# Performance work log

Hardware: AMD Instinct MI355X
Metric: run time of the kernel (lower is better)

The kernel has to match this reference:

```python
import jax, jax.numpy as jnp
from jax import lax
import numpy as np


def setup_inputs() -> dict:
    key = jax.random.key(0)
    k1, k2, k3, k4 = jax.random.split(key, 4)
    x = jax.random.normal(k1, (16, 128, 128, 128), dtype=jnp.float32)
    weight = jax.random.normal(k2, (128, 128, 3, 3), dtype=jnp.float32)      # ITPLConv.weight (d, c, kh, kw)
    depth_w = jax.random.normal(k3, (128,), dtype=jnp.float32)               # depthwise 1x1 conv weight (c,1,1,1) flattened
    point_w = jax.random.normal(k4, (128, 128), dtype=jnp.float32)           # pointwise 1x1 conv weight (out, in)
    return {"x": x, "weight": weight, "depth_w": depth_w, "point_w": point_w}


def reference(x, weight, depth_w, point_w):
    # ZeroPad2d(padding=1) on H and W
    xp = jnp.pad(x, ((0, 0), (0, 0), (1, 1), (1, 1)))
    # substract2: unfold(x) - x[:,:,:uh,:uw] broadcast, contracted with weight.
    # Algebraically: conv2d(xp, W, stride=1, VALID) - einsum(xp_crop, W.sum(kh,kw))
    conv = lax.conv_general_dilated(
        xp, weight, window_strides=(1, 1), padding="VALID",
        dimension_numbers=("NCHW", "OIHW", "NCHW"))
    uh, uw = conv.shape[2], conv.shape[3]
    wsum = jnp.sum(weight, axis=(2, 3))                      # (d, c)
    corr = jnp.einsum("nchw,dc->ndhw", xp[:, :, :uh, :uw], wsum)
    sub = conv - corr                                        # (n, d, uh, uw)
    # DWconv: depthwise 1x1 (per-channel scale) then pointwise 1x1
    y = sub * depth_w[None, :, None, None]
    out = jnp.einsum("nchw,oc->nohw", y, point_w)
    return out
```

## Files before the change

kernel.cpp:

```cpp
#include <hip/hip_runtime.h>
#include <hip/hip_bf16.h>


typedef __attribute__((ext_vector_type(8))) short bf16x8;
typedef __attribute__((ext_vector_type(4))) float f32x4;
typedef __attribute__((ext_vector_type(2))) unsigned int u32x2;

__device__ inline unsigned short f2bf(float f) {
    unsigned u = __builtin_bit_cast(unsigned, f);
    return (unsigned short)((u + 0x7FFFu + ((u >> 16) & 1u)) >> 16);
}

__device__ inline void gll16(const void* g, void* l) {
    __builtin_amdgcn_global_load_lds((const __attribute__((address_space(1))) void*)g,
                                     (__attribute__((address_space(3))) void*)l, 16, 0, 0);
}

__global__ void fuse_weights_bf16(const float* __restrict__ W,
                                  const float* __restrict__ dw,
                                  const float* __restrict__ P,
                                  unsigned short* __restrict__ w2b) {
    const int c = blockIdx.x;
    const int o = threadIdx.x;
    float acc[9];
#pragma unroll
    for (int t = 0; t < 9; ++t) acc[t] = 0.f;
    for (int d = 0; d < 128; ++d) {
        const float s = P[o * 128 + d] * dw[d];
        const float* wp = W + (size_t)(d * 128 + c) * 9;
        float tsum = 0.f;
#pragma unroll
        for (int t = 0; t < 9; ++t) {
            const float wv = wp[t];
            acc[t] = fmaf(s, wv, acc[t]);
            tsum += wv;
        }
        acc[0] = fmaf(-s, tsum, acc[0]);
    }
#pragma unroll
    for (int t = 0; t < 9; ++t)
        w2b[(t * 128 + o) * 128 + c] = f2bf(acc[t]);
}

__global__ __launch_bounds__(256) void to_nhwc_bf16(const float* __restrict__ x,
                                                    unsigned short* __restrict__ xb,
                                                    unsigned short* __restrict__ zrow) {
    __shared__ __attribute__((aligned(16))) unsigned ys[128 * 68];
    const int h = blockIdx.x, n = blockIdx.y, tid = (int)threadIdx.x;
    const int wv = tid >> 6, l = tid & 63;

#pragma unroll
    for (int i = 0; i < 4; ++i) {
        const int wh = (i & 1) * 64;
        const int CB0 = (2 * wv + (i >> 1)) * 16;
        const int c0 = CB0 + 4 * (l >> 4);
        const int w0 = wh + 4 * (l & 15);

        float4 v[4];
#pragma unroll
        for (int r = 0; r < 4; ++r)
            v[r] = *reinterpret_cast<const float4*>(
                x + ((((size_t)n * 128 + c0 + r) * 128 + h) * 128 + w0));

        const float* vf = reinterpret_cast<const float*>(v);
#pragma unroll
        for (int j = 0; j < 4; ++j) {
            unsigned u0 = (unsigned)f2bf(vf[0 * 4 + j]) | ((unsigned)f2bf(vf[1 * 4 + j]) << 16);
            unsigned u1 = (unsigned)f2bf(vf[2 * 4 + j]) | ((unsigned)f2bf(vf[3 * 4 + j]) << 16);
            u32x2 st; st[0] = u0; st[1] = u1;
            *reinterpret_cast<u32x2*>(&ys[(w0 + j) * 68 + (c0 >> 1)]) = st;
        }
    }
    __syncthreads();

#pragma unroll
    for (int k = 0; k < 8; ++k) {
        const int u = tid + 256 * k;
        const int c8 = u & 15, w = u >> 4;
        bf16x8 val = *reinterpret_cast<const bf16x8*>(
            reinterpret_cast<const unsigned short*>(ys) + w * 136 + c8 * 8);
        *reinterpret_cast<bf16x8*>(
            xb + ((((size_t)n * 128 + h) * 128 + w) * 128 + c8 * 8)) = val;
    }

    if (h == 0 && n == 0) {
        bf16x8 z = 0;
        for (int u = tid; u < 2048; u += 256)
            *reinterpret_cast<bf16x8*>(zrow + u * 8) = z;
    }
}

#define LDS_CHUNK (3 * 132 * 32)

__global__ __launch_bounds__(256, 2) void itpl_mfma_kernel(
    const unsigned short* __restrict__ xb,
    const unsigned short* __restrict__ w2b,
    const unsigned short* __restrict__ zrow,
    float* __restrict__ out) {
    __shared__ __attribute__((aligned(16))) unsigned short lds[2][LDS_CHUNK];

    const int bid = (int)blockIdx.x;
    const int lin = (bid & 7) * 256 + (bid >> 3);
    const int h = lin & 127, n = lin >> 7;

    const int tid = (int)threadIdx.x;
    const int l = tid & 63, wid = tid >> 6;
    const int wr = wid >> 1, wc = wid & 1;

    f32x4 acc[4][4];
#pragma unroll
    for (int i = 0; i < 4; ++i)
#pragma unroll
        for (int j = 0; j < 4; ++j) acc[i][j] = {0.f, 0.f, 0.f, 0.f};

    if (tid < 48) {
        const int slot = tid & 3, row = tid >> 2;
        const int buf = row / 6, rr = row % 6, r = rr >> 1, wi = (rr & 1) ? 129 : 0;
        bf16x8 z = 0;
        *reinterpret_cast<bf16x8*>(&lds[buf][(r * 132 + wi) * 32 + slot * 8]) = z;
    }

    const size_t nbase = (size_t)n * 128;

    auto stage = [&](int buf, int c0) {
        for (int s = wid * 6; s < wid * 6 + 6; ++s) {
            const int r = s >> 3, seg = s & 7;
            const int hr = h + r - 1;
            const int wl = seg * 16 + (l >> 2);
            const int wi = 1 + wl;
            const int q = (l & 3) ^ ((wi >> 1) & 3);
            const unsigned short* src;
            if ((unsigned)hr < 128u)
                src = xb + (((nbase + hr) * 128 + wl) * 128) + c0 + q * 8;
            else
                src = zrow + (wl * 128 + c0 + q * 8);
            gll16(src, (void*)&lds[buf][(r * 132 + 1 + seg * 16) * 32]);
        }
    };

    auto compute = [&](int buf, int c0) {
        const unsigned short* lb = &lds[buf][0];
#pragma unroll
        for (int r = 0; r < 3; ++r) {
            bf16x8 bfr[3][4];
#pragma unroll
            for (int tt = 0; tt < 3; ++tt)
#pragma unroll
                for (int ni = 0; ni < 4; ++ni) {
                    const int t = r * 3 + tt;
                    const int o = wc * 64 + ni * 16 + (l & 15);
                    bfr[tt][ni] = *reinterpret_cast<const bf16x8*>(
                        w2b + ((t * 128 + o) * 128 + c0 + (l >> 4) * 8));
                }
#pragma unroll
            for (int kw = 0; kw < 3; ++kw) {
                bf16x8 afr[4];
#pragma unroll
                for (int mi = 0; mi < 4; ++mi) {
                    const int wi = 1 + wr * 64 + mi * 16 + (l & 15) + kw - 1;
                    const int slot = (l >> 4) ^ ((wi >> 1) & 3);
                    afr[mi] = *reinterpret_cast<const bf16x8*>(
                        lb + (r * 132 + wi) * 32 + slot * 8);
                }
#pragma unroll
                for (int mi = 0; mi < 4; ++mi)
#pragma unroll
                    for (int ni = 0; ni < 4; ++ni)
                        acc[mi][ni] = __builtin_amdgcn_mfma_f32_16x16x32_bf16(
                            afr[mi], bfr[kw][ni], acc[mi][ni], 0, 0, 0);
            }
        }
    };

    stage(0, 0);
    __syncthreads();
#pragma unroll
    for (int k = 0; k < 4; ++k) {
        if (k < 3) stage((k + 1) & 1, (k + 1) * 32);
        compute(k & 1, k * 32);
        __syncthreads();
    }

    const size_t ob = (nbase * 128 + h) * 128;
#pragma unroll
    for (int mi = 0; mi < 4; ++mi) {
        const int w = wr * 64 + mi * 16 + (l >> 4) * 4;
#pragma unroll
        for (int ni = 0; ni < 4; ++ni) {
            const int o = wc * 64 + ni * 16 + (l & 15);
            *reinterpret_cast<f32x4*>(out + ob + (size_t)o * 128 * 128 + w) = acc[mi][ni];
        }
    }
}

#define CB 32
__global__ void fuse_weights_kernel(const float* __restrict__ W,
                                    const float* __restrict__ dw,
                                    const float* __restrict__ P,
                                    float* __restrict__ W2) {
    const int c = blockIdx.x;
    const int o = threadIdx.x;
    float acc[9];
#pragma unroll
    for (int t = 0; t < 9; ++t) acc[t] = 0.f;
    for (int d = 0; d < 128; ++d) {
        const float s = P[o * 128 + d] * dw[d];
        const float* wp = W + (size_t)(d * 128 + c) * 9;
        float tsum = 0.f;
#pragma unroll
        for (int t = 0; t < 9; ++t) {
            const float wv = wp[t];
            acc[t] = fmaf(s, wv, acc[t]);
            tsum += wv;
        }
        acc[0] = fmaf(-s, tsum, acc[0]);
    }
#pragma unroll
    for (int t = 0; t < 9; ++t) W2[(c * 9 + t) * 128 + o] = acc[t];
}

__global__ __launch_bounds__(256) void itpl_conv_kernel(const float* __restrict__ x,
                                                        const float* __restrict__ W2,
                                                        float* __restrict__ out) {
    __shared__ float xs[CB][3][132];
    const int h = blockIdx.x;
    const int n = blockIdx.y;
    const int tid = (int)threadIdx.x;
    const int pg = tid & 15;
    const int og = tid >> 4;
    float acc[8][8];
#pragma unroll
    for (int i = 0; i < 8; ++i)
#pragma unroll
        for (int p = 0; p < 8; ++p) acc[i][p] = 0.f;
    for (int c0 = 0; c0 < 128; c0 += CB) {
        __syncthreads();
        for (int g = tid; g < CB * 3 * 32; g += 256) {
            const int f4 = g & 31;
            const int row = g >> 5;
            const int r = row % 3;
            const int c = row / 3;
            const int hr = h + r - 1;
            float4 v = make_float4(0.f, 0.f, 0.f, 0.f);
            if ((unsigned)hr < 128u)
                v = *reinterpret_cast<const float4*>(
                    x + ((((size_t)n * 128 + c0 + c) * 128 + hr) * 128 + f4 * 4));
            float* dst = &xs[c][r][1 + f4 * 4];
            dst[0] = v.x; dst[1] = v.y; dst[2] = v.z; dst[3] = v.w;
        }
        if (tid < CB * 3) {
            const int r = tid % 3;
            const int c = tid / 3;
            xs[c][r][0] = 0.f;
            xs[c][r][129] = 0.f;
        }
        __syncthreads();
        for (int c = 0; c < CB; ++c) {
#pragma unroll
            for (int kh = 0; kh < 3; ++kh) {
                float xr[12];
                const float* xsp = &xs[c][kh][pg * 8];
                *reinterpret_cast<float4*>(&xr[0]) = *reinterpret_cast<const float4*>(xsp);
                *reinterpret_cast<float4*>(&xr[4]) = *reinterpret_cast<const float4*>(xsp + 4);
                *reinterpret_cast<float4*>(&xr[8]) = *reinterpret_cast<const float4*>(xsp + 8);
#pragma unroll
                for (int kw = 0; kw < 3; ++kw) {
                    const float* wp = W2 + (size_t)((c0 + c) * 9 + kh * 3 + kw) * 128 + og * 8;
                    float wv[8];
                    *reinterpret_cast<float4*>(&wv[0]) = *reinterpret_cast<const float4*>(wp);
                    *reinterpret_cast<float4*>(&wv[4]) = *reinterpret_cast<const float4*>(wp + 4);
#pragma unroll
                    for (int i = 0; i < 8; ++i)
#pragma unroll
                        for (int p = 0; p < 8; ++p)
                            acc[i][p] = fmaf(wv[i], xr[p + kw], acc[i][p]);
                }
            }
        }
    }
#pragma unroll
    for (int i = 0; i < 8; ++i) {
        float* op = out + ((((size_t)n * 128 + og * 8 + i) * 128 + h) * 128 + pg * 8);
        *reinterpret_cast<float4*>(op)     = make_float4(acc[i][0], acc[i][1], acc[i][2], acc[i][3]);
        *reinterpret_cast<float4*>(op + 4) = make_float4(acc[i][4], acc[i][5], acc[i][6], acc[i][7]);
    }
}

extern "C" void kernel_launch(void* const* d_in, const int* in_sizes, int n_in,
                              void* d_out, int out_size, void* d_ws, size_t ws_size,
                              hipStream_t stream) {
    const float* x  = (const float*)d_in[0];
    const float* W  = (const float*)d_in[1];
    const float* dw = (const float*)d_in[2];
    const float* P  = (const float*)d_in[3];
    float* out = (float*)d_out;

    const size_t XB_BYTES = 67108864ull;
    const size_t ZR_BYTES = 32768ull;
    const size_t W2B_BYTES = 294912ull;
    if (ws_size >= XB_BYTES + ZR_BYTES + W2B_BYTES) {
        unsigned short* xbw  = (unsigned short*)d_ws;
        unsigned short* zrow = (unsigned short*)((char*)d_ws + XB_BYTES);
        unsigned short* w2b  = (unsigned short*)((char*)d_ws + XB_BYTES + ZR_BYTES);
        fuse_weights_bf16<<<128, 128, 0, stream>>>(W, dw, P, w2b);
        to_nhwc_bf16<<<dim3(128, 16), 256, 0, stream>>>(x, xbw, zrow);
        itpl_mfma_kernel<<<2048, 256, 0, stream>>>(xbw, w2b, zrow, out);
    } else {
        float* W2 = (float*)d_ws;
        fuse_weights_kernel<<<128, 128, 0, stream>>>(W, dw, P, W2);
        itpl_conv_kernel<<<dim3(128, 16), 256, 0, stream>>>(x, W2, out);
    }
}
```

Before: 413.2 us.

## Merge prep kernels and retile MFMA conv to 512 threads with swapped operands

The weight-fusion and NHWC-conversion kernels are merged into one launch, and the weight fusion now stages W in shared memory and splits the reduction over d between two thread halves. The main MFMA kernel moves to 512 threads with 8 waves, each computing 64 output channels by 32 pixels, so the weight fragments become the A operand. Weights are stored in a layout grouped by 8 input channels so those fragment loads coalesce. This cuts launch overhead and per-wave register pressure to allow more waves in flight. The cost is output stores that become scalar strided writes along w instead of f32x4 vectors.

```diff
diff --git a/kernel.cpp b/kernel.cpp
--- a/kernel.cpp
+++ b/kernel.cpp
@@ -1,5 +1,4 @@
 #include <hip/hip_runtime.h>
-#include <hip/hip_bf16.h>
 
 
 typedef __attribute__((ext_vector_type(8))) short bf16x8;
@@ -16,85 +15,101 @@
                                      (__attribute__((address_space(3))) void*)l, 16, 0, 0);
 }
 
-__global__ void fuse_weights_bf16(const float* __restrict__ W,
-                                  const float* __restrict__ dw,
-                                  const float* __restrict__ P,
-                                  unsigned short* __restrict__ w2b) {
-    const int c = blockIdx.x;
-    const int o = threadIdx.x;
-    float acc[9];
-#pragma unroll
-    for (int t = 0; t < 9; ++t) acc[t] = 0.f;
-    for (int d = 0; d < 128; ++d) {
-        const float s = P[o * 128 + d] * dw[d];
-        const float* wp = W + (size_t)(d * 128 + c) * 9;
-        float tsum = 0.f;
-#pragma unroll
-        for (int t = 0; t < 9; ++t) {
-            const float wv = wp[t];
-            acc[t] = fmaf(s, wv, acc[t]);
-            tsum += wv;
-        }
-        acc[0] = fmaf(-s, tsum, acc[0]);
-    }
-#pragma unroll
-    for (int t = 0; t < 9; ++t)
-        w2b[(t * 128 + o) * 128 + c] = f2bf(acc[t]);
-}
-
-__global__ __launch_bounds__(256) void to_nhwc_bf16(const float* __restrict__ x,
-                                                    unsigned short* __restrict__ xb,
-                                                    unsigned short* __restrict__ zrow) {
-    __shared__ __attribute__((aligned(16))) unsigned ys[128 * 68];
-    const int h = blockIdx.x, n = blockIdx.y, tid = (int)threadIdx.x;
-    const int wv = tid >> 6, l = tid & 63;
-
-#pragma unroll
-    for (int i = 0; i < 4; ++i) {
-        const int wh = (i & 1) * 64;
-        const int CB0 = (2 * wv + (i >> 1)) * 16;
-        const int c0 = CB0 + 4 * (l >> 4);
-        const int w0 = wh + 4 * (l & 15);
-
-        float4 v[4];
-#pragma unroll
-        for (int r = 0; r < 4; ++r)
-            v[r] = *reinterpret_cast<const float4*>(
-                x + ((((size_t)n * 128 + c0 + r) * 128 + h) * 128 + w0));
-
-        const float* vf = reinterpret_cast<const float*>(v);
-#pragma unroll
-        for (int j = 0; j < 4; ++j) {
-            unsigned u0 = (unsigned)f2bf(vf[0 * 4 + j]) | ((unsigned)f2bf(vf[1 * 4 + j]) << 16);
-            unsigned u1 = (unsigned)f2bf(vf[2 * 4 + j]) | ((unsigned)f2bf(vf[3 * 4 + j]) << 16);
-            u32x2 st; st[0] = u0; st[1] = u1;
-            *reinterpret_cast<u32x2*>(&ys[(w0 + j) * 68 + (c0 >> 1)]) = st;
-        }
-    }
-    __syncthreads();
-
-#pragma unroll
-    for (int k = 0; k < 8; ++k) {
-        const int u = tid + 256 * k;
-        const int c8 = u & 15, w = u >> 4;
-        bf16x8 val = *reinterpret_cast<const bf16x8*>(
-            reinterpret_cast<const unsigned short*>(ys) + w * 136 + c8 * 8);
-        *reinterpret_cast<bf16x8*>(
-            xb + ((((size_t)n * 128 + h) * 128 + w) * 128 + c8 * 8)) = val;
-    }
-
-    if (h == 0 && n == 0) {
-        bf16x8 z = 0;
-        for (int u = tid; u < 2048; u += 256)
-            *reinterpret_cast<bf16x8*>(zrow + u * 8) = z;
+__global__ __launch_bounds__(256) void prep_kernel(
+    const float* __restrict__ x, const float* __restrict__ W,
+    const float* __restrict__ dw, const float* __restrict__ P,
+    unsigned short* __restrict__ xb, unsigned short* __restrict__ zrow,
+    unsigned short* __restrict__ w2f) {
+    __shared__ __attribute__((aligned(16))) unsigned smem[128 * 68];
+    const int bid = (int)blockIdx.x, tid = (int)threadIdx.x;
+
+    if (bid < 2048) {
+        const int h = bid & 127, n = bid >> 7;
+        const int wv = tid >> 6, l = tid & 63;
+#pragma unroll
+        for (int i = 0; i < 4; ++i) {
+            const int wh = (i & 1) * 64;
+            const int CB0 = (2 * wv + (i >> 1)) * 16;
+            const int c0 = CB0 + 4 * (l >> 4);
+            const int w0 = wh + 4 * (l & 15);
+            float4 v[4];
+#pragma unroll
+            for (int r = 0; r < 4; ++r)
+                v[r] = *reinterpret_cast<const float4*>(
+                    x + ((((size_t)n * 128 + c0 + r) * 128 + h) * 128 + w0));
+            const float* vf = reinterpret_cast<const float*>(v);
+#pragma unroll
+            for (int j = 0; j < 4; ++j) {
+                unsigned u0 = (unsigned)f2bf(vf[0 * 4 + j]) | ((unsigned)f2bf(vf[1 * 4 + j]) << 16);
+                unsigned u1 = (unsigned)f2bf(vf[2 * 4 + j]) | ((unsigned)f2bf(vf[3 * 4 + j]) << 16);
+                u32x2 st; st[0] = u0; st[1] = u1;
+                *reinterpret_cast<u32x2*>(&smem[(w0 + j) * 68 + (c0 >> 1)]) = st;
+            }
+        }
+        __syncthreads();
+#pragma unroll
+        for (int k = 0; k < 8; ++k) {
+            const int u = tid + 256 * k;
+            const int c8 = u & 15, w = u >> 4;
+            bf16x8 val = *reinterpret_cast<const bf16x8*>(
+                reinterpret_cast<const unsigned short*>(smem) + w * 136 + c8 * 8);
+            *reinterpret_cast<bf16x8*>(
+                xb + ((((size_t)n * 128 + h) * 128 + w) * 128 + c8 * 8)) = val;
+        }
+        if (h == 0 && n == 0) {
+            bf16x8 z = 0;
+            for (int u = tid; u < 2048; u += 256)
+                *reinterpret_cast<bf16x8*>(zrow + u * 8) = z;
+        }
+    } else {
+        const int c = bid - 2048;
+        float* Wl  = reinterpret_cast<float*>(smem);
+        float* red = reinterpret_cast<float*>(smem) + 1152;
+        for (int idx = tid; idx < 1152; idx += 256)
+            Wl[idx] = W[(size_t)((idx / 9) * 128 + c) * 9 + (idx % 9)];
+        __syncthreads();
+        const int t8 = tid >> 7, o = tid & 127;
+        float pr[64];
+#pragma unroll
+        for (int q = 0; q < 16; ++q)
+            *reinterpret_cast<float4*>(&pr[q * 4]) = *reinterpret_cast<const float4*>(
+                P + (size_t)o * 128 + t8 * 64 + q * 4);
+        float acc[9];
+#pragma unroll
+        for (int t = 0; t < 9; ++t) acc[t] = 0.f;
+        for (int dd = 0; dd < 64; ++dd) {
+            const int d = t8 * 64 + dd;
+            const float s = pr[dd] * dw[d];
+            const float* wp = Wl + d * 9;
+            float tsum = 0.f;
+#pragma unroll
+            for (int t = 0; t < 9; ++t) {
+                const float wv2 = wp[t];
+                acc[t] = fmaf(s, wv2, acc[t]);
+                tsum += wv2;
+            }
+            acc[0] = fmaf(-s, tsum, acc[0]);
+        }
+        if (t8 == 1) {
+#pragma unroll
+            for (int t = 0; t < 9; ++t) red[o * 10 + t] = acc[t];
+        }
+        __syncthreads();
+        if (t8 == 0) {
+#pragma unroll
+            for (int t = 0; t < 9; ++t) {
+                const float v = acc[t] + red[o * 10 + t];
+                w2f[(size_t)((t * 16 + (c >> 3)) * 128 + o) * 8 + (c & 7)] = f2bf(v);
+            }
+        }
     }
 }
 
 #define LDS_CHUNK (3 * 132 * 32)
 
-__global__ __launch_bounds__(256, 2) void itpl_mfma_kernel(
+__global__ __launch_bounds__(512, 6) void itpl_mfma_kernel(
     const unsigned short* __restrict__ xb,
-    const unsigned short* __restrict__ w2b,
+    const unsigned short* __restrict__ w2f,
     const unsigned short* __restrict__ zrow,
     float* __restrict__ out) {
     __shared__ __attribute__((aligned(16))) unsigned short lds[2][LDS_CHUNK];
@@ -105,13 +120,13 @@
 
     const int tid = (int)threadIdx.x;
     const int l = tid & 63, wid = tid >> 6;
-    const int wr = wid >> 1, wc = wid & 1;
-
-    f32x4 acc[4][4];
+    const int ws = wid & 3, wo = wid >> 2;
+
+    f32x4 acc[4][2];
 #pragma unroll
     for (int i = 0; i < 4; ++i)
 #pragma unroll
-        for (int j = 0; j < 4; ++j) acc[i][j] = {0.f, 0.f, 0.f, 0.f};
+        for (int j = 0; j < 2; ++j) acc[i][j] = {0.f, 0.f, 0.f, 0.f};
 
     if (tid < 48) {
         const int slot = tid & 3, row = tid >> 2;
@@ -123,7 +138,9 @@
     const size_t nbase = (size_t)n * 128;
 
     auto stage = [&](int buf, int c0) {
-        for (int s = wid * 6; s < wid * 6 + 6; ++s) {
+#pragma unroll
+        for (int i = 0; i < 3; ++i) {
+            const int s = wid * 3 + i;
             const int r = s >> 3, seg = s & 7;
             const int hr = h + r - 1;
             const int wl = seg * 16 + (l >> 2);
@@ -140,34 +157,33 @@
 
     auto compute = [&](int buf, int c0) {
         const unsigned short* lb = &lds[buf][0];
+        const int g0 = c0 >> 3;
 #pragma unroll
         for (int r = 0; r < 3; ++r) {
-            bf16x8 bfr[3][4];
-#pragma unroll
-            for (int tt = 0; tt < 3; ++tt)
-#pragma unroll
-                for (int ni = 0; ni < 4; ++ni) {
-                    const int t = r * 3 + tt;
-                    const int o = wc * 64 + ni * 16 + (l & 15);
-                    bfr[tt][ni] = *reinterpret_cast<const bf16x8*>(
-                        w2b + ((t * 128 + o) * 128 + c0 + (l >> 4) * 8));
-                }
 #pragma unroll
             for (int kw = 0; kw < 3; ++kw) {
-                bf16x8 afr[4];
-#pragma unroll
-                for (int mi = 0; mi < 4; ++mi) {
-                    const int wi = 1 + wr * 64 + mi * 16 + (l & 15) + kw - 1;
+                const int t = r * 3 + kw;
+                bf16x8 afr[2];
+#pragma unroll
+                for (int si = 0; si < 2; ++si) {
+                    const int wi = 1 + ws * 32 + si * 16 + (l & 15) + kw - 1;
                     const int slot = (l >> 4) ^ ((wi >> 1) & 3);
-                    afr[mi] = *reinterpret_cast<const bf16x8*>(
+                    afr[si] = *reinterpret_cast<const bf16x8*>(
                         lb + (r * 132 + wi) * 32 + slot * 8);
                 }
-#pragma unroll
-                for (int mi = 0; mi < 4; ++mi)
-#pragma unroll
-                    for (int ni = 0; ni < 4; ++ni)
-                        acc[mi][ni] = __builtin_amdgcn_mfma_f32_16x16x32_bf16(
-                            afr[mi], bfr[kw][ni], acc[mi][ni], 0, 0, 0);
+                bf16x8 bfr[4];
+#pragma unroll
+                for (int oi = 0; oi < 4; ++oi) {
+                    const int o = wo * 64 + oi * 16 + (l & 15);
+                    bfr[oi] = *reinterpret_cast<const bf16x8*>(
+                        w2f + (size_t)((t * 16 + g0 + (l >> 4)) * 128 + o) * 8);
+                }
+#pragma unroll
+                for (int oi = 0; oi < 4; ++oi)
+#pragma unroll
+                    for (int si = 0; si < 2; ++si)
+                        acc[oi][si] = __builtin_amdgcn_mfma_f32_16x16x32_bf16(
+                            bfr[oi], afr[si], acc[oi][si], 0, 0, 0);
             }
         }
     };
@@ -181,14 +197,16 @@
         __syncthreads();
     }
 
-    const size_t ob = (nbase * 128 + h) * 128;
-#pragma unroll
-    for (int mi = 0; mi < 4; ++mi) {
-        const int w = wr * 64 + mi * 16 + (l >> 4) * 4;
-#pragma unroll
-        for (int ni = 0; ni < 4; ++ni) {
-            const int o = wc * 64 + ni * 16 + (l & 15);
-            *reinterpret_cast<f32x4*>(out + ob + (size_t)o * 128 * 128 + w) = acc[mi][ni];
+    float* ob = out + nbase * 16384 + (size_t)h * 128;
+#pragma unroll
+    for (int oi = 0; oi < 4; ++oi) {
+        const int o0 = wo * 64 + oi * 16 + (l >> 4) * 4;
+#pragma unroll
+        for (int si = 0; si < 2; ++si) {
+            const int w = ws * 32 + si * 16 + (l & 15);
+#pragma unroll
+            for (int j = 0; j < 4; ++j)
+                ob[(size_t)(o0 + j) * 16384 + w] = acc[oi][si][j];
         }
     }
 }
@@ -301,10 +319,9 @@
     if (ws_size >= XB_BYTES + ZR_BYTES + W2B_BYTES) {
         unsigned short* xbw  = (unsigned short*)d_ws;
         unsigned short* zrow = (unsigned short*)((char*)d_ws + XB_BYTES);
-        unsigned short* w2b  = (unsigned short*)((char*)d_ws + XB_BYTES + ZR_BYTES);
-        fuse_weights_bf16<<<128, 128, 0, stream>>>(W, dw, P, w2b);
-        to_nhwc_bf16<<<dim3(128, 16), 256, 0, stream>>>(x, xbw, zrow);
-        itpl_mfma_kernel<<<2048, 256, 0, stream>>>(xbw, w2b, zrow, out);
+        unsigned short* w2f  = (unsigned short*)((char*)d_ws + XB_BYTES + ZR_BYTES);
+        prep_kernel<<<2176, 256, 0, stream>>>(x, W, dw, P, xbw, zrow, w2f);
+        itpl_mfma_kernel<<<2048, 512, 0, stream>>>(xbw, w2f, zrow, out);
     } else {
         float* W2 = (float*)d_ws;
         fuse_weights_kernel<<<128, 128, 0, stream>>>(W, dw, P, W2);
```

After: 345.0 us. 1.2x faster.
